# Optimization experiments

Measured on AMD Instinct MI355X. Metric: run time of the kernel, lower is better.

## Reference

```python
import jax, jax.numpy as jnp
import numpy as np

N_NODES = 50000
N_EDGES = 500000
D_IN = 128
D_HID = 128
D_OUT = 128
N_GRAPHS = 1024


def gcn_conv(x, W, b, row, col, n_nodes):
    # x: [N, d_in] -> [N, d_out]; PyG GCNConv with add_self_loops + symmetric norm
    h = x @ W  # [N, d_out]
    loops = jnp.arange(n_nodes, dtype=row.dtype)
    r = jnp.concatenate([row, loops])  # source
    c = jnp.concatenate([col, loops])  # target
    deg = jax.ops.segment_sum(jnp.ones(r.shape[0], dtype=x.dtype), c, num_segments=n_nodes)
    dinv = jnp.where(deg > 0, jax.lax.rsqrt(jnp.maximum(deg, 1.0)), 0.0)
    norm = dinv[r] * dinv[c]  # [E+N]
    msg = h[r] * norm[:, None]  # gather + scale
    out = jax.ops.segment_sum(msg, c, num_segments=n_nodes)  # scatter-add at targets
    return out + b


def setup_inputs() -> dict:
    key = jax.random.key(0)
    ks = jax.random.split(key, 10)
    x = jax.random.normal(ks[0], (N_NODES, D_IN), dtype=jnp.float32)
    edge_index = jax.random.randint(ks[1], (2, N_EDGES), 0, N_NODES, dtype=jnp.int64)
    batch = jnp.sort(jax.random.randint(ks[2], (N_NODES,), 0, N_GRAPHS, dtype=jnp.int64))
    s1 = 1.0 / np.sqrt(D_IN)
    s2 = 1.0 / np.sqrt(D_HID)
    W1 = jax.random.uniform(ks[3], (D_IN, D_HID), jnp.float32, -s1, s1)
    b1 = jnp.zeros((D_HID,), jnp.float32)
    W2 = jax.random.uniform(ks[4], (D_HID, D_HID), jnp.float32, -s2, s2)
    b2 = jnp.zeros((D_HID,), jnp.float32)
    Wf = jax.random.uniform(ks[5], (D_HID, D_OUT), jnp.float32, -s2, s2)
    bf = jax.random.uniform(ks[6], (D_OUT,), jnp.float32, -s2, s2)
    return {"x": x, "edge_index": edge_index, "batch": batch,
            "W1": W1, "b1": b1, "W2": W2, "b2": b2, "Wf": Wf, "bf": bf}


def reference(x, edge_index, batch, W1, b1, W2, b2, Wf, bf):
    n = x.shape[0]
    row, col = edge_index[0], edge_index[1]
    h = jax.nn.relu(gcn_conv(x, W1, b1, row, col, n))
    h = jax.nn.relu(gcn_conv(h, W2, b2, row, col, n))
    # global_mean_pool over graph ids
    sums = jax.ops.segment_sum(h, batch, num_segments=N_GRAPHS)  # [G, d]
    cnts = jax.ops.segment_sum(jnp.ones((n,), h.dtype), batch, num_segments=N_GRAPHS)
    pooled = sums / jnp.maximum(cnts, 1.0)[:, None]
    return pooled @ Wf + bf  # [G, D_OUT]
```

## Files before the change

### kernel.cpp

```cpp
#include <hip/hip_runtime.h>
#include <hip/hip_bf16.h>


#define D 128

typedef __attribute__((ext_vector_type(8))) short short8;
typedef __attribute__((ext_vector_type(4))) float f32x4;

__device__ __forceinline__ int swz(int row, int kbyte) {
    return row * 256 + (kbyte ^ ((row & 7) << 4));
}

__global__ __launch_bounds__(256) void k_init(int4* __restrict__ degcnt4, int n4, int zb,
                                              const float* __restrict__ W1,
                                              const float* __restrict__ W2,
                                              ushort* __restrict__ h1, ushort* __restrict__ l1,
                                              ushort* __restrict__ h2, ushort* __restrict__ l2) {
    int b = blockIdx.x;
    if (b < zb) {
        int i = b * 256 + threadIdx.x;
        if (i < n4) degcnt4[i] = make_int4(0, 0, 0, 0);
        return;
    }
    int bb = b - zb;
    const float* W = (bb < 8) ? W1 : W2;
    ushort* Wh = (bb < 8) ? h1 : h2;
    ushort* Wl = (bb < 8) ? l1 : l2;
    int t = (bb & 7) * 256 + threadIdx.x;
    int nrow = t >> 4;
    int kc = t & 15;
    uint hw[8], lw[8];
#pragma unroll
    for (int j = 0; j < 8; ++j) {
        float f = W[(kc * 8 + j) * D + nrow];
        uint ub = __float_as_uint(f);
        uint hb = ub & 0xffff0000u;
        float r = f - __uint_as_float(hb);
        hw[j] = hb >> 16;
        lw[j] = __float_as_uint(r) >> 16;
    }
    uint4 vh = make_uint4(hw[0] | (hw[1] << 16), hw[2] | (hw[3] << 16),
                          hw[4] | (hw[5] << 16), hw[6] | (hw[7] << 16));
    uint4 vl = make_uint4(lw[0] | (lw[1] << 16), lw[2] | (lw[3] << 16),
                          lw[4] | (lw[5] << 16), lw[6] | (lw[7] << 16));
    *(uint4*)&Wh[nrow * D + kc * 8] = vh;
    *(uint4*)&Wl[nrow * D + kc * 8] = vl;
}

__global__ void k_deg(const int* __restrict__ col, int* __restrict__ cnt, int E) {
    int e = (blockIdx.x * blockDim.x + threadIdx.x) * 4;
    if (e + 3 < E) {
        int4 c = *(const int4*)&col[e];
        atomicAdd(&cnt[c.x], 1);
        atomicAdd(&cnt[c.y], 1);
        atomicAdd(&cnt[c.z], 1);
        atomicAdd(&cnt[c.w], 1);
    } else {
        for (; e < E; ++e) atomicAdd(&cnt[col[e]], 1);
    }
}

__global__ __launch_bounds__(256) void k_scan_partial(const int* __restrict__ cnt,
                                                      int* __restrict__ partial, int n) {
    int t = threadIdx.x;
    int base = blockIdx.x * 1024 + t * 4;
    int s = 0;
#pragma unroll
    for (int j = 0; j < 4; ++j) {
        int i = base + j;
        if (i < n) s += cnt[i];
    }
#pragma unroll
    for (int o = 32; o > 0; o >>= 1) s += __shfl_down(s, o, 64);
    __shared__ int ws[4];
    if ((t & 63) == 0) ws[t >> 6] = s;
    __syncthreads();
    if (t == 0) partial[blockIdx.x] = ws[0] + ws[1] + ws[2] + ws[3];
}

__global__ __launch_bounds__(256) void k_scan_final(const int* __restrict__ cnt,
                                                    const int* __restrict__ partial,
                                                    int* __restrict__ offs,
                                                    int* __restrict__ cursor,
                                                    float* __restrict__ dinv,
                                                    int n, int E) {
    int t = threadIdx.x;
    int lane = t & 63;
    int base = blockIdx.x * 1024 + t * 4;
    int v[4];
    int s = 0;
#pragma unroll
    for (int j = 0; j < 4; ++j) {
        int i = base + j;
        v[j] = (i < n) ? cnt[i] : 0;
        s += v[j];
    }
    int inc = s;
#pragma unroll
    for (int o = 1; o < 64; o <<= 1) {
        int u = __shfl_up(inc, o, 64);
        if (lane >= o) inc += u;
    }
    __shared__ int wsum[4];
    __shared__ int bpref;
    if (lane == 63) wsum[t >> 6] = inc;
    if (t == 0) {
        int run = 0;
        for (int b = 0; b < blockIdx.x; ++b) run += partial[b];
        bpref = run;
        if (blockIdx.x == 0) offs[n] = E;
    }
    __syncthreads();
    int woff = 0;
    int w = t >> 6;
    for (int k = 0; k < w; ++k) woff += wsum[k];
    int excl = woff + (inc - s) + bpref;
#pragma unroll
    for (int j = 0; j < 4; ++j) {
        int i = base + j;
        if (i < n) {
            offs[i] = excl;
            cursor[i] = excl;
            dinv[i] = 1.0f / sqrtf((float)(v[j] + 1));
        }
        excl += v[j];
    }
}

__global__ void k_fill(const int* __restrict__ ei, int* __restrict__ cursor,
                       int* __restrict__ csr, int E) {
    int e = (blockIdx.x * blockDim.x + threadIdx.x) * 4;
    if (e + 3 < E) {
        int4 r = *(const int4*)&ei[e];
        int4 c = *(const int4*)&ei[E + e];
        int p0 = atomicAdd(&cursor[c.x], 1);
        int p1 = atomicAdd(&cursor[c.y], 1);
        int p2 = atomicAdd(&cursor[c.z], 1);
        int p3 = atomicAdd(&cursor[c.w], 1);
        csr[p0] = r.x;
        csr[p1] = r.y;
        csr[p2] = r.z;
        csr[p3] = r.w;
    } else {
        for (; e < E; ++e) {
            int rr = ei[e], cc = ei[E + e];
            int pos = atomicAdd(&cursor[cc], 1);
            csr[pos] = rr;
        }
    }
}

#define TM 128
template <bool ASLICED>
__global__ __launch_bounds__(512, 4) void k_gemm(const float* __restrict__ A,
                                                 const ushort* __restrict__ Bt_hi,
                                                 const ushort* __restrict__ Bt_lo,
                                                 const float* __restrict__ dinv,
                                                 float* __restrict__ C, int n) {
    extern __shared__ char lds[];
    char* Bh = lds;
    char* Bl = lds + 32 * 1024;

    int tid = threadIdx.x;
    int wave = tid >> 6, lane = tid & 63;
    int li = lane & 15, lg = lane >> 4;
    int row0 = blockIdx.x * TM;
    int grow = row0 + wave * 16 + li;
    bool valid = grow < n;

    float4 a[4][2];
#pragma unroll
    for (int ks = 0; ks < 4; ++ks) {
        int k0 = ks * 32 + lg * 8;
        if (valid) {
            const float4* p;
            if (ASLICED)
                p = (const float4*)(A + ((size_t)(k0 >> 4) * n + grow) * 16 + (k0 & 15));
            else
                p = (const float4*)(A + (size_t)grow * D + k0);
            a[ks][0] = p[0];
            a[ks][1] = p[1];
        } else {
            a[ks][0] = make_float4(0.f, 0.f, 0.f, 0.f);
            a[ks][1] = make_float4(0.f, 0.f, 0.f, 0.f);
        }
    }

#pragma unroll
    for (int it = tid; it < 2048; it += 512) {
        int r = it >> 4, kc = it & 15;
        uint4 vh = *(const uint4*)(Bt_hi + r * D + kc * 8);
        uint4 vl = *(const uint4*)(Bt_lo + r * D + kc * 8);
        *(uint4*)(Bh + swz(r, kc * 16)) = vh;
        *(uint4*)(Bl + swz(r, kc * 16)) = vl;
    }
    __syncthreads();

    short8 ah[4], al[4];
#pragma unroll
    for (int ks = 0; ks < 4; ++ks) {
        float f[8] = {a[ks][0].x, a[ks][0].y, a[ks][0].z, a[ks][0].w,
                      a[ks][1].x, a[ks][1].y, a[ks][1].z, a[ks][1].w};
#pragma unroll
        for (int j = 0; j < 8; ++j) {
            uint ub = __float_as_uint(f[j]);
            uint hb = ub & 0xffff0000u;
            float r = f[j] - __uint_as_float(hb);
            ah[ks][j] = (short)(hb >> 16);
            al[ks][j] = (short)(__float_as_uint(r) >> 16);
        }
    }

    f32x4 acc[8];
#pragma unroll
    for (int i = 0; i < 8; ++i) acc[i] = (f32x4){0.f, 0.f, 0.f, 0.f};

#pragma unroll
    for (int ks = 0; ks < 4; ++ks) {
        int kb = ks * 64 + lg * 16;
#pragma unroll
        for (int nt = 0; nt < 8; ++nt) {
            short8 bh = *(const short8*)(Bh + swz(nt * 16 + li, kb));
            short8 bl = *(const short8*)(Bl + swz(nt * 16 + li, kb));
            acc[nt] = __builtin_amdgcn_mfma_f32_16x16x32_bf16(ah[ks], bh, acc[nt], 0, 0, 0);
            acc[nt] = __builtin_amdgcn_mfma_f32_16x16x32_bf16(al[ks], bh, acc[nt], 0, 0, 0);
            acc[nt] = __builtin_amdgcn_mfma_f32_16x16x32_bf16(ah[ks], bl, acc[nt], 0, 0, 0);
        }
    }

    int crow0 = row0 + wave * 16 + lg * 4;
#pragma unroll
    for (int j = 0; j < 4; ++j) {
        int gr = crow0 + j;
        if (gr < n) {
            float dv = dinv[gr];
#pragma unroll
            for (int nt = 0; nt < 8; ++nt)
                C[((size_t)nt * n + gr) * 16 + li] = acc[nt][j] * dv;
        }
    }
}

#define AGG_NB 64
#define CSR_CAP 1152
__global__ __launch_bounds__(256) void k_agg(const float* __restrict__ hs,
                                             const float* __restrict__ dinv,
                                             const int* __restrict__ offs,
                                             const int* __restrict__ csr,
                                             const float* __restrict__ bias,
                                             float* __restrict__ outs, int n) {
    __shared__ int lofs[AGG_NB + 1];
    __shared__ int lcsr[CSR_CAP];
    int slice = blockIdx.x & 7;
    int chunk = blockIdx.x >> 3;
    int node0 = chunk * AGG_NB;
    int nend = node0 + AGG_NB; if (nend > n) nend = n;
    int nn = nend - node0;
    if (threadIdx.x <= nn) lofs[threadIdx.x] = offs[node0 + threadIdx.x];
    __syncthreads();
    int S = lofs[0];
    int span = lofs[nn] - S;
    bool uselds = (span <= CSR_CAP);
    if (uselds) {
        for (int i = threadIdx.x; i < span; i += 256) lcsr[i] = csr[S + i];
    }
    __syncthreads();

    int lnode = threadIdx.x >> 2;
    int node = node0 + lnode;
    if (node >= n) return;
    int l4 = (threadIdx.x & 3) * 4;

    const float* hbase = hs + (size_t)slice * n * 16;
    float di = dinv[node];
    int s = lofs[lnode] - S, e = lofs[lnode + 1] - S;
    f32x4 acc = *(const f32x4*)(hbase + (size_t)node * 16 + l4);
    if (uselds) {
        int p = s;
        for (; p + 8 <= e; p += 8) {
            int r0 = lcsr[p],     r1 = lcsr[p + 1], r2 = lcsr[p + 2], r3 = lcsr[p + 3];
            int r4 = lcsr[p + 4], r5 = lcsr[p + 5], r6 = lcsr[p + 6], r7 = lcsr[p + 7];
            f32x4 h0 = *(const f32x4*)(hbase + (size_t)r0 * 16 + l4);
            f32x4 h1 = *(const f32x4*)(hbase + (size_t)r1 * 16 + l4);
            f32x4 h2 = *(const f32x4*)(hbase + (size_t)r2 * 16 + l4);
            f32x4 h3 = *(const f32x4*)(hbase + (size_t)r3 * 16 + l4);
            f32x4 h4 = *(const f32x4*)(hbase + (size_t)r4 * 16 + l4);
            f32x4 h5 = *(const f32x4*)(hbase + (size_t)r5 * 16 + l4);
            f32x4 h6 = *(const f32x4*)(hbase + (size_t)r6 * 16 + l4);
            f32x4 h7 = *(const f32x4*)(hbase + (size_t)r7 * 16 + l4);
            acc += ((h0 + h1) + (h2 + h3)) + ((h4 + h5) + (h6 + h7));
        }
        for (; p + 4 <= e; p += 4) {
            int r0 = lcsr[p], r1 = lcsr[p + 1], r2 = lcsr[p + 2], r3 = lcsr[p + 3];
            f32x4 h0 = *(const f32x4*)(hbase + (size_t)r0 * 16 + l4);
            f32x4 h1 = *(const f32x4*)(hbase + (size_t)r1 * 16 + l4);
            f32x4 h2 = *(const f32x4*)(hbase + (size_t)r2 * 16 + l4);
            f32x4 h3 = *(const f32x4*)(hbase + (size_t)r3 * 16 + l4);
            acc += (h0 + h1) + (h2 + h3);
        }
        for (; p < e; ++p)
            acc += *(const f32x4*)(hbase + (size_t)lcsr[p] * 16 + l4);
    } else {
        const int* gcsr = csr + S;
        int p = s;
        for (; p + 4 <= e; p += 4) {
            int r0 = gcsr[p], r1 = gcsr[p + 1], r2 = gcsr[p + 2], r3 = gcsr[p + 3];
            f32x4 h0 = *(const f32x4*)(hbase + (size_t)r0 * 16 + l4);
            f32x4 h1 = *(const f32x4*)(hbase + (size_t)r1 * 16 + l4);
            f32x4 h2 = *(const f32x4*)(hbase + (size_t)r2 * 16 + l4);
            f32x4 h3 = *(const f32x4*)(hbase + (size_t)r3 * 16 + l4);
            acc += (h0 + h1) + (h2 + h3);
        }
        for (; p < e; ++p)
            acc += *(const f32x4*)(hbase + (size_t)gcsr[p] * 16 + l4);
    }
    f32x4 b4 = *(const f32x4*)(bias + slice * 16 + l4);
    f32x4 v;
#pragma unroll
    for (int j = 0; j < 4; ++j) v[j] = fmaxf(acc[j] * di + b4[j], 0.f);
    __builtin_nontemporal_store(v, (f32x4*)(outs + ((size_t)slice * n + node) * 16 + l4));
}

__global__ __launch_bounds__(128) void k_poolfinal(const float* __restrict__ hs,
                                                   const int* __restrict__ batch, int n,
                                                   const float* __restrict__ Wf,
                                                   const float* __restrict__ bf,
                                                   float* __restrict__ out) {
    __shared__ int sse[2];
    int g = blockIdx.x;
    if (threadIdx.x == 0) {
        int lo = 0, hi = n;
        while (lo < hi) { int m = (lo + hi) >> 1; if (batch[m] < g) lo = m + 1; else hi = m; }
        sse[0] = lo;
    } else if (threadIdx.x == 64) {
        int lo = 0, hi = n;
        while (lo < hi) { int m = (lo + hi) >> 1; if (batch[m] < g + 1) lo = m + 1; else hi = m; }
        sse[1] = lo;
    }
    __syncthreads();
    int s = sse[0], e = sse[1];

    int q = threadIdx.x & 31;
    int r = threadIdx.x >> 5;
    int slice = q >> 2;
    int l4 = (q & 3) * 4;
    const float* base = hs + (size_t)slice * n * 16 + l4;
    f32x4 acc = (f32x4){0.f, 0.f, 0.f, 0.f};
    for (int i = s + r; i < e; i += 4)
        acc += *(const f32x4*)(base + (size_t)i * 16);

    __shared__ f32x4 red[128];
    __shared__ float pr[D];
    red[threadIdx.x] = acc;
    __syncthreads();
    if (threadIdx.x < 32) {
        f32x4 t = (red[q] + red[q + 32]) + (red[q + 64] + red[q + 96]);
        float cnt = (float)(e - s);
        if (cnt < 1.f) cnt = 1.f;
#pragma unroll
        for (int j = 0; j < 4; ++j) pr[q * 4 + j] = t[j] / cnt;
    }
    __syncthreads();
    int d = threadIdx.x;
    float o = bf[d];
#pragma unroll 8
    for (int k = 0; k < D; ++k) o += pr[k] * Wf[k * D + d];
    out[g * D + d] = o;
}

extern "C" void kernel_launch(void* const* d_in, const int* in_sizes, int n_in,
                              void* d_out, int out_size, void* d_ws, size_t ws_size,
                              hipStream_t stream) {
    const float* x  = (const float*)d_in[0];
    const int*   ei = (const int*)d_in[1];
    const int*   bt = (const int*)d_in[2];
    const float* W1 = (const float*)d_in[3];
    const float* b1 = (const float*)d_in[4];
    const float* W2 = (const float*)d_in[5];
    const float* b2 = (const float*)d_in[6];
    const float* Wf = (const float*)d_in[7];
    const float* bf = (const float*)d_in[8];
    float* out = (float*)d_out;

    int n = in_sizes[2];
    int E = in_sizes[1] / 2;
    int G = out_size / D;

    char* w = (char*)d_ws;
    size_t off = 0;
    auto alloc = [&](size_t bytes) -> void* {
        void* p = w + off;
        off = (off + bytes + 511) & ~(size_t)511;
        return p;
    };
    int*    degcnt = (int*)alloc((size_t)n * 4);
    int*    cursor = (int*)alloc((size_t)n * 4);
    int*    offs   = (int*)alloc((size_t)(n + 1) * 4);
    float*  dinv   = (float*)alloc((size_t)n * 4);
    int*    csr    = (int*)alloc((size_t)E * 4);
    float*  hw     = (float*)alloc((size_t)n * D * 4);
    float*  ha     = (float*)alloc((size_t)n * D * 4);
    int*    partial= (int*)alloc((size_t)256 * 4);
    ushort* wt1h   = (ushort*)alloc((size_t)D * D * 2);
    ushort* wt1l   = (ushort*)alloc((size_t)D * D * 2);
    ushort* wt2h   = (ushort*)alloc((size_t)D * D * 2);
    ushort* wt2l   = (ushort*)alloc((size_t)D * D * 2);

    int n4 = (n + 3) / 4;
    int zb = (n4 + 255) / 256;
    k_init<<<zb + 16, 256, 0, stream>>>((int4*)degcnt, n4, zb,
                                        W1, W2, wt1h, wt1l, wt2h, wt2l);

    int e4b = (E / 4 + 255) / 256 + 1;
    int sb = (n + 1023) / 1024;
    k_deg<<<e4b, 256, 0, stream>>>(ei + E, degcnt, E);
    k_scan_partial<<<sb, 256, 0, stream>>>(degcnt, partial, n);
    k_scan_final<<<sb, 256, 0, stream>>>(degcnt, partial, offs, cursor, dinv, n, E);
    k_fill<<<e4b, 256, 0, stream>>>(ei, cursor, csr, E);

    int gb = (n + TM - 1) / TM;
    int ab = 8 * ((n + AGG_NB - 1) / AGG_NB);
    size_t lds_bytes = 64 * 1024;

    k_gemm<false><<<gb, 512, lds_bytes, stream>>>(x, wt1h, wt1l, dinv, hw, n);
    k_agg<<<ab, 256, 0, stream>>>(hw, dinv, offs, csr, b1, ha, n);
    k_gemm<true><<<gb, 512, lds_bytes, stream>>>(ha, wt2h, wt2l, dinv, hw, n);
    k_agg<<<ab, 256, 0, stream>>>(hw, dinv, offs, csr, b2, ha, n);
    k_poolfinal<<<G, 128, 0, stream>>>(ha, bt, n, Wf, bf, out);
}
```

Baseline: 164.5 us.

## Fuse mean-pool into second aggregation via segmented atomics, enlarge agg blocks

The second aggregation kernel now reduces its per-node outputs directly into per-graph pooled sums. It does this with an in-block segmented reduction over the sorted batch ids followed by float atomicAdds, so the second-layer activations are never written back and reread. The pooled buffer is zeroed in the init kernel, and the final kernel now only divides by the counts and applies the output linear layer. Aggregation blocks double to 128 nodes and 512 threads with a larger LDS CSR cache. The change adds atomic contention and makes the float summation order nondeterministic.

```diff
diff --git a/kernel.cpp b/kernel.cpp
--- a/kernel.cpp
+++ b/kernel.cpp
@@ -12,6 +12,7 @@
 }
 
 __global__ __launch_bounds__(256) void k_init(int4* __restrict__ degcnt4, int n4, int zb,
+                                              int4* __restrict__ pooled4, int p4, int pb,
                                               const float* __restrict__ W1,
                                               const float* __restrict__ W2,
                                               ushort* __restrict__ h1, ushort* __restrict__ l1,
@@ -22,7 +23,12 @@
         if (i < n4) degcnt4[i] = make_int4(0, 0, 0, 0);
         return;
     }
-    int bb = b - zb;
+    if (b < zb + pb) {
+        int i = (b - zb) * 256 + threadIdx.x;
+        if (i < p4) pooled4[i] = make_int4(0, 0, 0, 0);
+        return;
+    }
+    int bb = b - zb - pb;
     const float* W = (bb < 8) ? W1 : W2;
     ushort* Wh = (bb < 8) ? h1 : h2;
     ushort* Wl = (bb < 8) ? l1 : l2;
@@ -241,92 +247,121 @@
     }
 }
 
-#define AGG_NB 64
-#define CSR_CAP 1152
-__global__ __launch_bounds__(256) void k_agg(const float* __restrict__ hs,
+#define AGG_NB 128
+#define CSR_CAP 2304
+template <bool POOL>
+__global__ __launch_bounds__(512) void k_agg(const float* __restrict__ hs,
                                              const float* __restrict__ dinv,
                                              const int* __restrict__ offs,
                                              const int* __restrict__ csr,
                                              const float* __restrict__ bias,
-                                             float* __restrict__ outs, int n) {
+                                             float* __restrict__ outs,
+                                             const int* __restrict__ batch,
+                                             float* __restrict__ pooled, int n) {
     __shared__ int lofs[AGG_NB + 1];
     __shared__ int lcsr[CSR_CAP];
+    __shared__ f32x4 arr[POOL ? AGG_NB : 1][4];
+    __shared__ int gid[POOL ? AGG_NB : 1];
+
     int slice = blockIdx.x & 7;
     int chunk = blockIdx.x >> 3;
     int node0 = chunk * AGG_NB;
     int nend = node0 + AGG_NB; if (nend > n) nend = n;
     int nn = nend - node0;
-    if (threadIdx.x <= nn) lofs[threadIdx.x] = offs[node0 + threadIdx.x];
+    if ((int)threadIdx.x <= nn) lofs[threadIdx.x] = offs[node0 + threadIdx.x];
     __syncthreads();
     int S = lofs[0];
     int span = lofs[nn] - S;
     bool uselds = (span <= CSR_CAP);
     if (uselds) {
-        for (int i = threadIdx.x; i < span; i += 256) lcsr[i] = csr[S + i];
+        for (int i = threadIdx.x; i < span; i += 512) lcsr[i] = csr[S + i];
     }
     __syncthreads();
 
     int lnode = threadIdx.x >> 2;
     int node = node0 + lnode;
-    if (node >= n) return;
-    int l4 = (threadIdx.x & 3) * 4;
+    bool act = node < n;
+    int l4q = threadIdx.x & 3;
+    int l4 = l4q * 4;
 
     const float* hbase = hs + (size_t)slice * n * 16;
-    float di = dinv[node];
-    int s = lofs[lnode] - S, e = lofs[lnode + 1] - S;
-    f32x4 acc = *(const f32x4*)(hbase + (size_t)node * 16 + l4);
-    if (uselds) {
-        int p = s;
-        for (; p + 8 <= e; p += 8) {
-            int r0 = lcsr[p],     r1 = lcsr[p + 1], r2 = lcsr[p + 2], r3 = lcsr[p + 3];
-            int r4 = lcsr[p + 4], r5 = lcsr[p + 5], r6 = lcsr[p + 6], r7 = lcsr[p + 7];
-            f32x4 h0 = *(const f32x4*)(hbase + (size_t)r0 * 16 + l4);
-            f32x4 h1 = *(const f32x4*)(hbase + (size_t)r1 * 16 + l4);
-            f32x4 h2 = *(const f32x4*)(hbase + (size_t)r2 * 16 + l4);
-            f32x4 h3 = *(const f32x4*)(hbase + (size_t)r3 * 16 + l4);
-            f32x4 h4 = *(const f32x4*)(hbase + (size_t)r4 * 16 + l4);
-            f32x4 h5 = *(const f32x4*)(hbase + (size_t)r5 * 16 + l4);
-            f32x4 h6 = *(const f32x4*)(hbase + (size_t)r6 * 16 + l4);
-            f32x4 h7 = *(const f32x4*)(hbase + (size_t)r7 * 16 + l4);
-            acc += ((h0 + h1) + (h2 + h3)) + ((h4 + h5) + (h6 + h7));
-        }
-        for (; p + 4 <= e; p += 4) {
-            int r0 = lcsr[p], r1 = lcsr[p + 1], r2 = lcsr[p + 2], r3 = lcsr[p + 3];
-            f32x4 h0 = *(const f32x4*)(hbase + (size_t)r0 * 16 + l4);
-            f32x4 h1 = *(const f32x4*)(hbase + (size_t)r1 * 16 + l4);
-            f32x4 h2 = *(const f32x4*)(hbase + (size_t)r2 * 16 + l4);
-            f32x4 h3 = *(const f32x4*)(hbase + (size_t)r3 * 16 + l4);
-            acc += (h0 + h1) + (h2 + h3);
-        }
-        for (; p < e; ++p)
-            acc += *(const f32x4*)(hbase + (size_t)lcsr[p] * 16 + l4);
+    f32x4 v = (f32x4){0.f, 0.f, 0.f, 0.f};
+    if (act) {
+        float di = dinv[node];
+        int s = lofs[lnode] - S, e = lofs[lnode + 1] - S;
+        f32x4 acc = *(const f32x4*)(hbase + (size_t)node * 16 + l4);
+        if (uselds) {
+            int p = s;
+            for (; p + 8 <= e; p += 8) {
+                int r0 = lcsr[p],     r1 = lcsr[p + 1], r2 = lcsr[p + 2], r3 = lcsr[p + 3];
+                int r4 = lcsr[p + 4], r5 = lcsr[p + 5], r6 = lcsr[p + 6], r7 = lcsr[p + 7];
+                f32x4 h0 = *(const f32x4*)(hbase + (size_t)r0 * 16 + l4);
+                f32x4 h1 = *(const f32x4*)(hbase + (size_t)r1 * 16 + l4);
+                f32x4 h2 = *(const f32x4*)(hbase + (size_t)r2 * 16 + l4);
+                f32x4 h3 = *(const f32x4*)(hbase + (size_t)r3 * 16 + l4);
+                f32x4 h4 = *(const f32x4*)(hbase + (size_t)r4 * 16 + l4);
+                f32x4 h5 = *(const f32x4*)(hbase + (size_t)r5 * 16 + l4);
+                f32x4 h6 = *(const f32x4*)(hbase + (size_t)r6 * 16 + l4);
+                f32x4 h7 = *(const f32x4*)(hbase + (size_t)r7 * 16 + l4);
+                acc += ((h0 + h1) + (h2 + h3)) + ((h4 + h5) + (h6 + h7));
+            }
+            for (; p + 4 <= e; p += 4) {
+                int r0 = lcsr[p], r1 = lcsr[p + 1], r2 = lcsr[p + 2], r3 = lcsr[p + 3];
+                f32x4 h0 = *(const f32x4*)(hbase + (size_t)r0 * 16 + l4);
+                f32x4 h1 = *(const f32x4*)(hbase + (size_t)r1 * 16 + l4);
+                f32x4 h2 = *(const f32x4*)(hbase + (size_t)r2 * 16 + l4);
+                f32x4 h3 = *(const f32x4*)(hbase + (size_t)r3 * 16 + l4);
+                acc += (h0 + h1) + (h2 + h3);
+            }
+            for (; p < e; ++p)
+                acc += *(const f32x4*)(hbase + (size_t)lcsr[p] * 16 + l4);
+        } else {
+            const int* gcsr = csr + S;
+            int p = s;
+            for (; p + 4 <= e; p += 4) {
+                int r0 = gcsr[p], r1 = gcsr[p + 1], r2 = gcsr[p + 2], r3 = gcsr[p + 3];
+                f32x4 h0 = *(const f32x4*)(hbase + (size_t)r0 * 16 + l4);
+                f32x4 h1 = *(const f32x4*)(hbase + (size_t)r1 * 16 + l4);
+                f32x4 h2 = *(const f32x4*)(hbase + (size_t)r2 * 16 + l4);
+                f32x4 h3 = *(const f32x4*)(hbase + (size_t)r3 * 16 + l4);
+                acc += (h0 + h1) + (h2 + h3);
+            }
+            for (; p < e; ++p)
+                acc += *(const f32x4*)(hbase + (size_t)gcsr[p] * 16 + l4);
+        }
+        f32x4 b4 = *(const f32x4*)(bias + slice * 16 + l4);
+#pragma unroll
+        for (int j = 0; j < 4; ++j) v[j] = fmaxf(acc[j] * di + b4[j], 0.f);
+    }
+
+    if constexpr (!POOL) {
+        if (act)
+            __builtin_nontemporal_store(v, (f32x4*)(outs + ((size_t)slice * n + node) * 16 + l4));
     } else {
-        const int* gcsr = csr + S;
-        int p = s;
-        for (; p + 4 <= e; p += 4) {
-            int r0 = gcsr[p], r1 = gcsr[p + 1], r2 = gcsr[p + 2], r3 = gcsr[p + 3];
-            f32x4 h0 = *(const f32x4*)(hbase + (size_t)r0 * 16 + l4);
-            f32x4 h1 = *(const f32x4*)(hbase + (size_t)r1 * 16 + l4);
-            f32x4 h2 = *(const f32x4*)(hbase + (size_t)r2 * 16 + l4);
-            f32x4 h3 = *(const f32x4*)(hbase + (size_t)r3 * 16 + l4);
-            acc += (h0 + h1) + (h2 + h3);
-        }
-        for (; p < e; ++p)
-            acc += *(const f32x4*)(hbase + (size_t)gcsr[p] * 16 + l4);
-    }
-    f32x4 b4 = *(const f32x4*)(bias + slice * 16 + l4);
-    f32x4 v;
-#pragma unroll
-    for (int j = 0; j < 4; ++j) v[j] = fmaxf(acc[j] * di + b4[j], 0.f);
-    __builtin_nontemporal_store(v, (f32x4*)(outs + ((size_t)slice * n + node) * 16 + l4));
-}
-
-__global__ __launch_bounds__(128) void k_poolfinal(const float* __restrict__ hs,
-                                                   const int* __restrict__ batch, int n,
-                                                   const float* __restrict__ Wf,
-                                                   const float* __restrict__ bf,
-                                                   float* __restrict__ out) {
+        arr[lnode][l4q] = v;
+        if (l4q == 0) gid[lnode] = act ? batch[node] : -1;
+        __syncthreads();
+        if (act && (lnode == 0 || gid[lnode] != gid[lnode - 1])) {
+            int g = gid[lnode];
+            f32x4 ps = (f32x4){0.f, 0.f, 0.f, 0.f};
+            int j = lnode;
+            while (j < nn && gid[j] == g) { ps += arr[j][l4q]; ++j; }
+            float* pp = pooled + (size_t)g * D + slice * 16 + l4;
+            atomicAdd(pp + 0, ps[0]);
+            atomicAdd(pp + 1, ps[1]);
+            atomicAdd(pp + 2, ps[2]);
+            atomicAdd(pp + 3, ps[3]);
+        }
+    }
+}
+
+__global__ __launch_bounds__(128) void k_final(const float* __restrict__ pooled,
+                                               const int* __restrict__ batch, int n,
+                                               const float* __restrict__ Wf,
+                                               const float* __restrict__ bf,
+                                               float* __restrict__ out) {
     __shared__ int sse[2];
+    __shared__ float pr[D];
     int g = blockIdx.x;
     if (threadIdx.x == 0) {
         int lo = 0, hi = n;
@@ -338,30 +373,11 @@
         sse[1] = lo;
     }
     __syncthreads();
-    int s = sse[0], e = sse[1];
-
-    int q = threadIdx.x & 31;
-    int r = threadIdx.x >> 5;
-    int slice = q >> 2;
-    int l4 = (q & 3) * 4;
-    const float* base = hs + (size_t)slice * n * 16 + l4;
-    f32x4 acc = (f32x4){0.f, 0.f, 0.f, 0.f};
-    for (int i = s + r; i < e; i += 4)
-        acc += *(const f32x4*)(base + (size_t)i * 16);
-
-    __shared__ f32x4 red[128];
-    __shared__ float pr[D];
-    red[threadIdx.x] = acc;
-    __syncthreads();
-    if (threadIdx.x < 32) {
-        f32x4 t = (red[q] + red[q + 32]) + (red[q + 64] + red[q + 96]);
-        float cnt = (float)(e - s);
-        if (cnt < 1.f) cnt = 1.f;
-#pragma unroll
-        for (int j = 0; j < 4; ++j) pr[q * 4 + j] = t[j] / cnt;
-    }
-    __syncthreads();
+    float cnt = (float)(sse[1] - sse[0]);
+    if (cnt < 1.f) cnt = 1.f;
     int d = threadIdx.x;
+    pr[d] = pooled[(size_t)g * D + d] / cnt;
+    __syncthreads();
     float o = bf[d];
 #pragma unroll 8
     for (int k = 0; k < D; ++k) o += pr[k] * Wf[k * D + d];
@@ -400,6 +416,7 @@
     int*    csr    = (int*)alloc((size_t)E * 4);
     float*  hw     = (float*)alloc((size_t)n * D * 4);
     float*  ha     = (float*)alloc((size_t)n * D * 4);
+    float*  pooled = (float*)alloc((size_t)G * D * 4);
     int*    partial= (int*)alloc((size_t)256 * 4);
     ushort* wt1h   = (ushort*)alloc((size_t)D * D * 2);
     ushort* wt1l   = (ushort*)alloc((size_t)D * D * 2);
@@ -408,8 +425,11 @@
 
     int n4 = (n + 3) / 4;
     int zb = (n4 + 255) / 256;
-    k_init<<<zb + 16, 256, 0, stream>>>((int4*)degcnt, n4, zb,
-                                        W1, W2, wt1h, wt1l, wt2h, wt2l);
+    int p4 = (G * D + 3) / 4;
+    int pb = (p4 + 255) / 256;
+    k_init<<<zb + pb + 16, 256, 0, stream>>>((int4*)degcnt, n4, zb,
+                                             (int4*)pooled, p4, pb,
+                                             W1, W2, wt1h, wt1l, wt2h, wt2l);
 
     int e4b = (E / 4 + 255) / 256 + 1;
     int sb = (n + 1023) / 1024;
@@ -423,8 +443,8 @@
     size_t lds_bytes = 64 * 1024;
 
     k_gemm<false><<<gb, 512, lds_bytes, stream>>>(x, wt1h, wt1l, dinv, hw, n);
-    k_agg<<<ab, 256, 0, stream>>>(hw, dinv, offs, csr, b1, ha, n);
+    k_agg<false><<<ab, 512, 0, stream>>>(hw, dinv, offs, csr, b1, ha, bt, nullptr, n);
     k_gemm<true><<<gb, 512, lds_bytes, stream>>>(ha, wt2h, wt2l, dinv, hw, n);
-    k_agg<<<ab, 256, 0, stream>>>(hw, dinv, offs, csr, b2, ha, n);
-    k_poolfinal<<<G, 128, 0, stream>>>(ha, bt, n, Wf, bf, out);
-}
+    k_agg<true><<<ab, 512, 0, stream>>>(hw, dinv, offs, csr, b2, nullptr, bt, pooled, n);
+    k_final<<<G, 128, 0, stream>>>(pooled, bt, n, Wf, bf, out);
+}
```

Measured after the change: 179.2 us. 1.09x slower.
